# Performance work log

Measured on AMD Instinct MI355X. Metric: run time of the kernel, lower is better.

## Reference

```python
import jax, jax.numpy as jnp
import numpy as np
import math

CS = 8       # cell_size
NBINS = 8
SIGMA = 1.0
IMG = 224
BATCH = 256
TWO_PI = 2.0 * math.pi


def setup_inputs() -> dict:
    key = jax.random.key(0)
    x = jax.random.normal(key, (BATCH, 3, IMG, IMG), dtype=jnp.float32)
    coords = jnp.arange(CS, dtype=jnp.float32) - (CS - 1) / 2.0
    xx, yy = jnp.meshgrid(coords, coords, indexing='ij')
    gauss = jnp.exp(-(xx ** 2 + yy ** 2) / (2.0 * SIGMA ** 2)).reshape(1, CS * CS)
    kx = jnp.array([[-1., 0., 1.], [-2., 0., 2.], [-1., 0., 1.]], dtype=jnp.float32).reshape(1, 1, 3, 3)
    ky = jnp.array([[-1., -2., -1.], [0., 0., 0.], [1., 2., 1.]], dtype=jnp.float32).reshape(1, 1, 3, 3)
    return {"x": x, "gauss": gauss, "kx": kx, "ky": ky}


def _conv(im, k):
    # NCHW conv, padding=1, stride=1 (matches F.conv2d(..., padding=1))
    return jax.lax.conv_general_dilated(
        im, k, window_strides=(1, 1), padding=[(1, 1), (1, 1)],
        dimension_numbers=('NCHW', 'OIHW', 'NCHW'))


def reference(x, gauss, kx, ky):
    bs, _, H, W = x.shape
    gray = 0.2989 * x[:, 0:1] + 0.587 * x[:, 1:2] + 0.114 * x[:, 2:3]  # [bs,1,H,W]
    gx = _conv(gray, kx)
    gy = _conv(gray, ky)
    mag = jnp.sqrt(gx ** 2 + gy ** 2 + 1e-6)
    ang = jnp.mod(jnp.arctan2(gy, gx), TWO_PI)
    Hc, Wc = H // CS, W // CS
    n_cells = Hc * Wc

    def to_cells(a):
        # [bs,1,H,W] -> [bs*n_cells, CS*CS], within-cell order (kh,kw) row-major
        # matching F.unfold's kernel-position ordering.
        return a.reshape(bs, Hc, CS, Wc, CS).transpose(0, 1, 3, 2, 4).reshape(bs * n_cells, CS * CS)

    mags = to_cells(mag) * gauss  # gauss broadcasts over kernel positions
    angs = to_cells(ang)

    bin_w = TWO_PI / NBINS
    idx = (angs / bin_w).astype(jnp.int32) % NBINS  # [bs*n_cells, CS*CS]

    N = bs * n_cells
    hist = jnp.zeros((N, NBINS), dtype=mags.dtype)
    hist = hist.at[jnp.arange(N)[:, None], idx].add(mags)  # scatter_add per cell
    hist = hist.reshape(bs, n_cells * NBINS)
    hist = hist / (jnp.linalg.norm(hist, axis=1, keepdims=True) + 1e-6)
    return hist
```

## Files before the change

kernel.cpp:

```cpp
#include <hip/hip_runtime.h>
#include <math.h>

#define CS 8
#define NBINS 8
#define IMG 224
#define HC 28
#define OUTPER (HC*HC*NBINS)
#define BATCH 256
#define RS 16
#define GR (RS + 2)
#define GSTRIDE 232
#define GOFF 4

__global__ void hog_zero_kernel(float* __restrict__ sumsq) {
    if (threadIdx.x < BATCH) sumsq[threadIdx.x] = 0.f;
}

__global__ __launch_bounds__(256) void hog_hist_kernel(
    const float* __restrict__ x, const float* __restrict__ gauss,
    float* __restrict__ out, float* __restrict__ sumsq)
{
    const int b   = blockIdx.x;
    const int by  = blockIdx.y;
    const int tid = threadIdx.x;
    const int r0  = by * RS;

    __shared__ float g[GR][GSTRIDE];
    __shared__ float wsum[4];

    const size_t plane = (size_t)IMG * IMG;
    const float* xb = x + (size_t)b * 3 * plane;

    if (tid < GR * 2) {
        int rr = tid >> 1, cc = (tid & 1) ? (GOFF + IMG) : (GOFF - 1);
        g[rr][cc] = 0.f;
    }

    for (int idx = tid; idx < GR * (IMG / 4); idx += 256) {
        int row = idx / (IMG / 4), c4 = idx % (IMG / 4);
        int gr = r0 - 1 + row;
        float4 val = make_float4(0.f, 0.f, 0.f, 0.f);
        if (gr >= 0 && gr < IMG) {
            const float* base = xb + (size_t)gr * IMG;
            float4 R = ((const float4*)base)[c4];
            float4 G = ((const float4*)(base + plane))[c4];
            float4 B = ((const float4*)(base + 2 * plane))[c4];
            val.x = 0.2989f * R.x + 0.587f * G.x + 0.114f * B.x;
            val.y = 0.2989f * R.y + 0.587f * G.y + 0.114f * B.y;
            val.z = 0.2989f * R.z + 0.587f * G.z + 0.114f * B.z;
            val.w = 0.2989f * R.w + 0.587f * G.w + 0.114f * B.w;
        }
        *(float4*)&g[row][GOFF + c4 * 4] = val;
    }
    __syncthreads();

    float ssq = 0.f;
    if (tid < IMG) {
        const int c  = tid;
        const int wc = c & 7;

        float wgt[8];
        #pragma unroll
        for (int i = 0; i < 8; ++i) wgt[i] = gauss[i * 8 + wc];

        float h[8];
        #pragma unroll
        for (int k = 0; k < 8; ++k) h[k] = 0.f;

        auto dump = [&](int crow) {
            #pragma unroll
            for (int s = 1; s < 8; s <<= 1) {
                #pragma unroll
                for (int k = 0; k < 8; ++k) h[k] += __shfl_xor(h[k], s, 64);
            }
            float v = (wc < 4) ? ((wc < 2) ? (wc == 0 ? h[0] : h[1])
                                          : (wc == 2 ? h[2] : h[3]))
                               : ((wc < 6) ? (wc == 4 ? h[4] : h[5])
                                          : (wc == 6 ? h[6] : h[7]));
            out[(size_t)b * OUTPER + (size_t)crow * (HC * NBINS) + c] = v;
            ssq += v * v;
            #pragma unroll
            for (int k = 0; k < 8; ++k) h[k] = 0.f;
        };

        float t0 = g[0][c + 3], t1 = g[0][c + 4], t2 = g[0][c + 5];
        float m0 = g[1][c + 3], m1 = g[1][c + 4], m2 = g[1][c + 5];

        #pragma unroll
        for (int sr = 0; sr < RS; ++sr) {
            float b0 = g[sr + 2][c + 3], b1 = g[sr + 2][c + 4], b2 = g[sr + 2][c + 5];
            float gx = (t2 - t0) + 2.f * (m2 - m0) + (b2 - b0);
            float gy = (b0 - t0) + 2.f * (b1 - t1) + (b2 - t2);
            float mag = sqrtf(gx * gx + gy * gy + 1e-6f);
            float ax = fabsf(gx), ay = fabsf(gy);

            int bin;
            if (gy > 0.f)       bin = (gx > 0.f)  ? ((gy < gx) ? 0 : 1)
                                    : (gx == 0.f) ? 2 : ((ay > ax) ? 2 : 3);
            else if (gy == 0.f) bin = (gx < 0.f) ? 4 : 0;
            else                bin = (gx < 0.f)  ? ((ay < ax) ? 4 : 5)
                                    : (gx == 0.f) ? 6 : ((ay > ax) ? 6 : 7);

            float wm = wgt[sr & 7] * mag;
            #pragma unroll
            for (int k = 0; k < 8; ++k) h[k] += (bin == k) ? wm : 0.f;

            t0 = m0; t1 = m1; t2 = m2;
            m0 = b0; m1 = b1; m2 = b2;

            if (sr == 7)       dump(2 * by);
            else if (sr == 15) dump(2 * by + 1);
        }
    }

    #pragma unroll
    for (int o = 32; o > 0; o >>= 1) ssq += __shfl_down(ssq, o, 64);
    if ((tid & 63) == 0) wsum[tid >> 6] = ssq;
    __syncthreads();
    if (tid == 0) atomicAdd(&sumsq[b], wsum[0] + wsum[1] + wsum[2] + wsum[3]);
}

__global__ __launch_bounds__(256) void hog_norm_kernel(
    float* __restrict__ out, const float* __restrict__ sumsq)
{
    int i = blockIdx.x * blockDim.x + threadIdx.x;
    const int vec_per_img = OUTPER / 4;
    if (i >= BATCH * vec_per_img) return;
    int b = i / vec_per_img;
    float n = sqrtf(sumsq[b]) + 1e-6f;
    float4* o4 = (float4*)out;
    float4 v = o4[i];
    v.x /= n; v.y /= n; v.z /= n; v.w /= n;
    o4[i] = v;
}

extern "C" void kernel_launch(void* const* d_in, const int* in_sizes, int n_in,
                              void* d_out, int out_size, void* d_ws, size_t ws_size,
                              hipStream_t stream) {
    const float* x     = (const float*)d_in[0];
    const float* gauss = (const float*)d_in[1];
    float* out   = (float*)d_out;
    float* sumsq = (float*)d_ws;

    hog_zero_kernel<<<1, 256, 0, stream>>>(sumsq);
    dim3 grid(BATCH, IMG / RS);
    hog_hist_kernel<<<grid, 256, 0, stream>>>(x, gauss, out, sumsq);
    hog_norm_kernel<<<(BATCH * OUTPER / 4 + 255) / 256, 256, 0, stream>>>(out, sumsq);
}
```

Baseline: 244.4 us.

## Split grayscale into separate pass, double row strip height, use reciprocal normalization

Adds a standalone kernel that converts RGB to grayscale into workspace memory and also zeroes the per-image sum-of-squares, so the histogram kernel reads one gray plane instead of three colour planes. The histogram kernel now processes 32-row strips, halving the grid and the relative halo overhead, and loads tiles with a fixed unrolled loop using clamped addresses. Normalization multiplies by a reciprocal instead of dividing. The cost is an extra full-size gray write and read through global memory, plus fewer blocks per image.

Result: slower. 261.4 us (+7.0%).

```diff
diff --git a/kernel.cpp b/kernel.cpp
--- a/kernel.cpp
+++ b/kernel.cpp
@@ -7,17 +7,34 @@
 #define HC 28
 #define OUTPER (HC*HC*NBINS)
 #define BATCH 256
-#define RS 16
+#define P4 (IMG*IMG/4)
+#define RS 32
 #define GR (RS + 2)
 #define GSTRIDE 232
 #define GOFF 4
 
-__global__ void hog_zero_kernel(float* __restrict__ sumsq) {
-    if (threadIdx.x < BATCH) sumsq[threadIdx.x] = 0.f;
+__global__ __launch_bounds__(256) void hog_gray_kernel(
+    const float4* __restrict__ x, float4* __restrict__ gray,
+    float* __restrict__ sumsq)
+{
+    if (blockIdx.x == 0) sumsq[threadIdx.x] = 0.f;
+    int p = blockIdx.x * 256 + threadIdx.x;
+    int b = p / P4;
+    int i = p - b * P4;
+    const float4* xb = x + (size_t)b * 3 * P4;
+    float4 R = xb[i];
+    float4 G = xb[P4 + i];
+    float4 B = xb[2 * P4 + i];
+    float4 g;
+    g.x = 0.2989f * R.x + 0.587f * G.x + 0.114f * B.x;
+    g.y = 0.2989f * R.y + 0.587f * G.y + 0.114f * B.y;
+    g.z = 0.2989f * R.z + 0.587f * G.z + 0.114f * B.z;
+    g.w = 0.2989f * R.w + 0.587f * G.w + 0.114f * B.w;
+    gray[p] = g;
 }
 
 __global__ __launch_bounds__(256) void hog_hist_kernel(
-    const float* __restrict__ x, const float* __restrict__ gauss,
+    const float* __restrict__ gray, const float* __restrict__ gauss,
     float* __restrict__ out, float* __restrict__ sumsq)
 {
     const int b   = blockIdx.x;
@@ -28,29 +45,22 @@
     __shared__ float g[GR][GSTRIDE];
     __shared__ float wsum[4];
 
-    const size_t plane = (size_t)IMG * IMG;
-    const float* xb = x + (size_t)b * 3 * plane;
-
     if (tid < GR * 2) {
         int rr = tid >> 1, cc = (tid & 1) ? (GOFF + IMG) : (GOFF - 1);
         g[rr][cc] = 0.f;
     }
 
-    for (int idx = tid; idx < GR * (IMG / 4); idx += 256) {
-        int row = idx / (IMG / 4), c4 = idx % (IMG / 4);
-        int gr = r0 - 1 + row;
-        float4 val = make_float4(0.f, 0.f, 0.f, 0.f);
-        if (gr >= 0 && gr < IMG) {
-            const float* base = xb + (size_t)gr * IMG;
-            float4 R = ((const float4*)base)[c4];
-            float4 G = ((const float4*)(base + plane))[c4];
-            float4 B = ((const float4*)(base + 2 * plane))[c4];
-            val.x = 0.2989f * R.x + 0.587f * G.x + 0.114f * B.x;
-            val.y = 0.2989f * R.y + 0.587f * G.y + 0.114f * B.y;
-            val.z = 0.2989f * R.z + 0.587f * G.z + 0.114f * B.z;
-            val.w = 0.2989f * R.w + 0.587f * G.w + 0.114f * B.w;
-        }
-        *(float4*)&g[row][GOFF + c4 * 4] = val;
+    const float4* gb = (const float4*)(gray + (size_t)b * IMG * IMG);
+    #pragma unroll
+    for (int k = 0; k < 8; ++k) {
+        int idx = tid + k * 256;
+        int ii  = idx < GR * 56 ? idx : GR * 56 - 1;
+        int row = ii / 56, c4 = ii - row * 56;
+        int gr  = r0 - 1 + row;
+        int grc = gr < 0 ? 0 : (gr > IMG - 1 ? IMG - 1 : gr);
+        float4 v = gb[grc * 56 + c4];
+        if (gr < 0 || gr >= IMG) v = make_float4(0.f, 0.f, 0.f, 0.f);
+        if (idx < GR * 56) *(float4*)&g[row][GOFF + c4 * 4] = v;
     }
     __syncthreads();
 
@@ -108,8 +118,7 @@
             t0 = m0; t1 = m1; t2 = m2;
             m0 = b0; m1 = b1; m2 = b2;
 
-            if (sr == 7)       dump(2 * by);
-            else if (sr == 15) dump(2 * by + 1);
+            if ((sr & 7) == 7) dump(4 * by + (sr >> 3));
         }
     }
 
@@ -127,10 +136,10 @@
     const int vec_per_img = OUTPER / 4;
     if (i >= BATCH * vec_per_img) return;
     int b = i / vec_per_img;
-    float n = sqrtf(sumsq[b]) + 1e-6f;
+    float inv = 1.0f / (sqrtf(sumsq[b]) + 1e-6f);
     float4* o4 = (float4*)out;
     float4 v = o4[i];
-    v.x /= n; v.y /= n; v.z /= n; v.w /= n;
+    v.x *= inv; v.y *= inv; v.z *= inv; v.w *= inv;
     o4[i] = v;
 }
 
@@ -141,9 +150,11 @@
     const float* gauss = (const float*)d_in[1];
     float* out   = (float*)d_out;
     float* sumsq = (float*)d_ws;
+    float* gray  = (float*)d_ws + 256;
 
-    hog_zero_kernel<<<1, 256, 0, stream>>>(sumsq);
+    hog_gray_kernel<<<BATCH * P4 / 256, 256, 0, stream>>>(
+        (const float4*)x, (float4*)gray, sumsq);
     dim3 grid(BATCH, IMG / RS);
-    hog_hist_kernel<<<grid, 256, 0, stream>>>(x, gauss, out, sumsq);
+    hog_hist_kernel<<<grid, 256, 0, stream>>>(gray, gauss, out, sumsq);
     hog_norm_kernel<<<(BATCH * OUTPER / 4 + 255) / 256, 256, 0, stream>>>(out, sumsq);
 }
```

## Stream 56-row strips through ring buffer with prefetched loads, drop atomics

Applied to the files above, without the earlier changes.

Each block now handles a 56-row strip (7 cell rows) instead of 16 rows, using a 16-slot ring buffer in shared memory. While the current cell row is being computed, the next 8 gray rows are loaded into registers and written into the ring afterwards. This cuts halo reloads from 18/16 to 58/56 rows and overlaps global loads with compute. The per-image sum-of-squares now goes into per-strip partial slots instead of atomics, removing the zero kernel, and the norm kernel multiplies by a reciprocal. The trade-offs are fewer blocks (1024 instead of 3584), an extra barrier per cell row, and higher register pressure.

After: 236.5 us. 1.03x faster.

```diff
diff --git a/kernel.cpp b/kernel.cpp
--- a/kernel.cpp
+++ b/kernel.cpp
@@ -1,115 +1,146 @@
 #include <hip/hip_runtime.h>
 #include <math.h>
 
-#define CS 8
 #define NBINS 8
 #define IMG 224
 #define HC 28
 #define OUTPER (HC*HC*NBINS)
 #define BATCH 256
-#define RS 16
-#define GR (RS + 2)
+#define PL4 12544
 #define GSTRIDE 232
 #define GOFF 4
+#define SLOTS 16
 
-__global__ void hog_zero_kernel(float* __restrict__ sumsq) {
-    if (threadIdx.x < BATCH) sumsq[threadIdx.x] = 0.f;
-}
+__global__ __launch_bounds__(256) void hog_main_kernel(
+    const float4* __restrict__ x, const float* __restrict__ gauss,
+    float* __restrict__ out, float* __restrict__ partial)
+{
+    const int b     = blockIdx.x;
+    const int by    = blockIdx.y;
+    const int tid   = threadIdx.x;
+    const int rbase = by * 56;
 
-__global__ __launch_bounds__(256) void hog_hist_kernel(
-    const float* __restrict__ x, const float* __restrict__ gauss,
-    float* __restrict__ out, float* __restrict__ sumsq)
-{
-    const int b   = blockIdx.x;
-    const int by  = blockIdx.y;
-    const int tid = threadIdx.x;
-    const int r0  = by * RS;
-
-    __shared__ float g[GR][GSTRIDE];
+    __shared__ float g[SLOTS][GSTRIDE];
     __shared__ float wsum[4];
 
-    const size_t plane = (size_t)IMG * IMG;
-    const float* xb = x + (size_t)b * 3 * plane;
+    const float4* xb = x + (size_t)b * 3 * PL4;
 
-    if (tid < GR * 2) {
+    if (tid < SLOTS * 2) {
         int rr = tid >> 1, cc = (tid & 1) ? (GOFF + IMG) : (GOFF - 1);
         g[rr][cc] = 0.f;
     }
 
-    for (int idx = tid; idx < GR * (IMG / 4); idx += 256) {
-        int row = idx / (IMG / 4), c4 = idx % (IMG / 4);
-        int gr = r0 - 1 + row;
-        float4 val = make_float4(0.f, 0.f, 0.f, 0.f);
-        if (gr >= 0 && gr < IMG) {
-            const float* base = xb + (size_t)gr * IMG;
-            float4 R = ((const float4*)base)[c4];
-            float4 G = ((const float4*)(base + plane))[c4];
-            float4 B = ((const float4*)(base + 2 * plane))[c4];
-            val.x = 0.2989f * R.x + 0.587f * G.x + 0.114f * B.x;
-            val.y = 0.2989f * R.y + 0.587f * G.y + 0.114f * B.y;
-            val.z = 0.2989f * R.z + 0.587f * G.z + 0.114f * B.z;
-            val.w = 0.2989f * R.w + 0.587f * G.w + 0.114f * B.w;
+    {
+        float4 R[3], G[3], B[3];
+        int gr[3], c4[3]; bool act[3];
+        #pragma unroll
+        for (int k = 0; k < 3; ++k) {
+            int idx = tid + k * 256;
+            act[k] = idx < 560;
+            int ii = act[k] ? idx : 0;
+            int row = ii / 56; c4[k] = ii - row * 56;
+            gr[k] = rbase - 1 + row;
+            int grc = gr[k] < 0 ? 0 : (gr[k] > IMG - 1 ? IMG - 1 : gr[k]);
+            const float4* p = xb + grc * 56 + c4[k];
+            R[k] = p[0]; G[k] = p[PL4]; B[k] = p[2 * PL4];
         }
-        *(float4*)&g[row][GOFF + c4 * 4] = val;
+        #pragma unroll
+        for (int k = 0; k < 3; ++k) if (act[k]) {
+            bool z = (gr[k] < 0) || (gr[k] > IMG - 1);
+            float4 v;
+            v.x = z ? 0.f : 0.2989f * R[k].x + 0.587f * G[k].x + 0.114f * B[k].x;
+            v.y = z ? 0.f : 0.2989f * R[k].y + 0.587f * G[k].y + 0.114f * B[k].y;
+            v.z = z ? 0.f : 0.2989f * R[k].z + 0.587f * G[k].z + 0.114f * B[k].z;
+            v.w = z ? 0.f : 0.2989f * R[k].w + 0.587f * G[k].w + 0.114f * B[k].w;
+            *(float4*)&g[gr[k] & (SLOTS - 1)][GOFF + 4 * c4[k]] = v;
+        }
     }
     __syncthreads();
 
+    const int c = tid, wc = tid & 7;
+    float wgt[8];
+    #pragma unroll
+    for (int i = 0; i < 8; ++i) wgt[i] = gauss[i * 8 + wc];
     float ssq = 0.f;
-    if (tid < IMG) {
-        const int c  = tid;
-        const int wc = c & 7;
 
-        float wgt[8];
-        #pragma unroll
-        for (int i = 0; i < 8; ++i) wgt[i] = gauss[i * 8 + wc];
+    for (int s = 0; s < 7; ++s) {
+        float4 Rp[2], Gp[2], Bp[2];
+        int pgr[2], pc4[2]; bool pact[2];
+        if (s < 6) {
+            #pragma unroll
+            for (int k = 0; k < 2; ++k) {
+                int idx = tid + k * 256;
+                pact[k] = idx < 448;
+                int ii = pact[k] ? idx : 0;
+                int row = ii / 56; pc4[k] = ii - row * 56;
+                pgr[k] = rbase + 8 * s + 9 + row;
+                int grc = pgr[k] > IMG - 1 ? IMG - 1 : pgr[k];
+                const float4* p = xb + grc * 56 + pc4[k];
+                Rp[k] = p[0]; Gp[k] = p[PL4]; Bp[k] = p[2 * PL4];
+            }
+        }
 
-        float h[8];
-        #pragma unroll
-        for (int k = 0; k < 8; ++k) h[k] = 0.f;
+        if (tid < IMG) {
+            const int r0 = rbase + 8 * s;
+            float h[8];
+            #pragma unroll
+            for (int k = 0; k < 8; ++k) h[k] = 0.f;
 
-        auto dump = [&](int crow) {
+            int st = (r0 - 1) & (SLOTS - 1), sm = r0 & (SLOTS - 1);
+            float t0 = g[st][c + 3], t1 = g[st][c + 4], t2 = g[st][c + 5];
+            float m0 = g[sm][c + 3], m1 = g[sm][c + 4], m2 = g[sm][c + 5];
+
             #pragma unroll
-            for (int s = 1; s < 8; s <<= 1) {
+            for (int sr = 0; sr < 8; ++sr) {
+                int sb = (r0 + sr + 1) & (SLOTS - 1);
+                float b0 = g[sb][c + 3], b1 = g[sb][c + 4], b2 = g[sb][c + 5];
+                float gx = (t2 - t0) + 2.f * (m2 - m0) + (b2 - b0);
+                float gy = (b0 - t0) + 2.f * (b1 - t1) + (b2 - t2);
+                float mag = sqrtf(gx * gx + gy * gy + 1e-6f);
+                float ax = fabsf(gx), ay = fabsf(gy);
+
+                int bin;
+                if (gy > 0.f)       bin = (gx > 0.f)  ? ((gy < gx) ? 0 : 1)
+                                        : (gx == 0.f) ? 2 : ((ay > ax) ? 2 : 3);
+                else if (gy == 0.f) bin = (gx < 0.f) ? 4 : 0;
+                else                bin = (gx < 0.f)  ? ((ay < ax) ? 4 : 5)
+                                        : (gx == 0.f) ? 6 : ((ay > ax) ? 6 : 7);
+
+                float wm = wgt[sr] * mag;
                 #pragma unroll
-                for (int k = 0; k < 8; ++k) h[k] += __shfl_xor(h[k], s, 64);
+                for (int k = 0; k < 8; ++k) h[k] += (bin == k) ? wm : 0.f;
+
+                t0 = m0; t1 = m1; t2 = m2;
+                m0 = b0; m1 = b1; m2 = b2;
+            }
+
+            #pragma unroll
+            for (int sh = 1; sh < 8; sh <<= 1) {
+                #pragma unroll
+                for (int k = 0; k < 8; ++k) h[k] += __shfl_xor(h[k], sh, 64);
             }
             float v = (wc < 4) ? ((wc < 2) ? (wc == 0 ? h[0] : h[1])
                                           : (wc == 2 ? h[2] : h[3]))
                                : ((wc < 6) ? (wc == 4 ? h[4] : h[5])
                                           : (wc == 6 ? h[6] : h[7]));
+            int crow = by * 7 + s;
             out[(size_t)b * OUTPER + (size_t)crow * (HC * NBINS) + c] = v;
             ssq += v * v;
+        }
+        __syncthreads();
+
+        if (s < 6) {
             #pragma unroll
-            for (int k = 0; k < 8; ++k) h[k] = 0.f;
-        };
-
-        float t0 = g[0][c + 3], t1 = g[0][c + 4], t2 = g[0][c + 5];
-        float m0 = g[1][c + 3], m1 = g[1][c + 4], m2 = g[1][c + 5];
-
-        #pragma unroll
-        for (int sr = 0; sr < RS; ++sr) {
-            float b0 = g[sr + 2][c + 3], b1 = g[sr + 2][c + 4], b2 = g[sr + 2][c + 5];
-            float gx = (t2 - t0) + 2.f * (m2 - m0) + (b2 - b0);
-            float gy = (b0 - t0) + 2.f * (b1 - t1) + (b2 - t2);
-            float mag = sqrtf(gx * gx + gy * gy + 1e-6f);
-            float ax = fabsf(gx), ay = fabsf(gy);
-
-            int bin;
-            if (gy > 0.f)       bin = (gx > 0.f)  ? ((gy < gx) ? 0 : 1)
-                                    : (gx == 0.f) ? 2 : ((ay > ax) ? 2 : 3);
-            else if (gy == 0.f) bin = (gx < 0.f) ? 4 : 0;
-            else                bin = (gx < 0.f)  ? ((ay < ax) ? 4 : 5)
-                                    : (gx == 0.f) ? 6 : ((ay > ax) ? 6 : 7);
-
-            float wm = wgt[sr & 7] * mag;
-            #pragma unroll
-            for (int k = 0; k < 8; ++k) h[k] += (bin == k) ? wm : 0.f;
-
-            t0 = m0; t1 = m1; t2 = m2;
-            m0 = b0; m1 = b1; m2 = b2;
-
-            if (sr == 7)       dump(2 * by);
-            else if (sr == 15) dump(2 * by + 1);
+            for (int k = 0; k < 2; ++k) if (pact[k]) {
+                bool z = pgr[k] > IMG - 1;
+                float4 v;
+                v.x = z ? 0.f : 0.2989f * Rp[k].x + 0.587f * Gp[k].x + 0.114f * Bp[k].x;
+                v.y = z ? 0.f : 0.2989f * Rp[k].y + 0.587f * Gp[k].y + 0.114f * Bp[k].y;
+                v.z = z ? 0.f : 0.2989f * Rp[k].z + 0.587f * Gp[k].z + 0.114f * Bp[k].z;
+                v.w = z ? 0.f : 0.2989f * Rp[k].w + 0.587f * Gp[k].w + 0.114f * Bp[k].w;
+                *(float4*)&g[pgr[k] & (SLOTS - 1)][GOFF + 4 * pc4[k]] = v;
+            }
+            __syncthreads();
         }
     }
 
@@ -117,20 +148,22 @@
     for (int o = 32; o > 0; o >>= 1) ssq += __shfl_down(ssq, o, 64);
     if ((tid & 63) == 0) wsum[tid >> 6] = ssq;
     __syncthreads();
-    if (tid == 0) atomicAdd(&sumsq[b], wsum[0] + wsum[1] + wsum[2] + wsum[3]);
+    if (tid == 0) partial[by * BATCH + b] = wsum[0] + wsum[1] + wsum[2] + wsum[3];
 }
 
 __global__ __launch_bounds__(256) void hog_norm_kernel(
-    float* __restrict__ out, const float* __restrict__ sumsq)
+    float* __restrict__ out, const float* __restrict__ partial)
 {
     int i = blockIdx.x * blockDim.x + threadIdx.x;
     const int vec_per_img = OUTPER / 4;
     if (i >= BATCH * vec_per_img) return;
     int b = i / vec_per_img;
-    float n = sqrtf(sumsq[b]) + 1e-6f;
+    float s = partial[b] + partial[BATCH + b] + partial[2 * BATCH + b]
+            + partial[3 * BATCH + b];
+    float inv = 1.0f / (sqrtf(s) + 1e-6f);
     float4* o4 = (float4*)out;
     float4 v = o4[i];
-    v.x /= n; v.y /= n; v.z /= n; v.w /= n;
+    v.x *= inv; v.y *= inv; v.z *= inv; v.w *= inv;
     o4[i] = v;
 }
 
@@ -139,11 +172,11 @@
                               hipStream_t stream) {
     const float* x     = (const float*)d_in[0];
     const float* gauss = (const float*)d_in[1];
-    float* out   = (float*)d_out;
-    float* sumsq = (float*)d_ws;
+    float* out     = (float*)d_out;
+    float* partial = (float*)d_ws;
 
-    hog_zero_kernel<<<1, 256, 0, stream>>>(sumsq);
-    dim3 grid(BATCH, IMG / RS);
-    hog_hist_kernel<<<grid, 256, 0, stream>>>(x, gauss, out, sumsq);
-    hog_norm_kernel<<<(BATCH * OUTPER / 4 + 255) / 256, 256, 0, stream>>>(out, sumsq);
+    dim3 grid(BATCH, 4);
+    hog_main_kernel<<<grid, 256, 0, stream>>>(
+        (const float4*)x, gauss, out, partial);
+    hog_norm_kernel<<<(BATCH * OUTPER / 4 + 255) / 256, 256, 0, stream>>>(out, partial);
 }
```

## Assign one cell row per wave, drop atomics and zero kernel

Applied to the files above, without the earlier changes.

Restructures the histogram kernel so each 64-lane wave owns one 8-row cell strip with its own LDS tile, using wave barriers instead of block syncs. Every column is handled by a lane across four chunks, so all 64 lanes stay busy rather than only 224 of 256 threads. Per-strip sums of squares are written to a partial buffer rather than accumulated with atomics, which removes the zeroing kernel. The normalization kernel runs one block per image, reduces the partials and multiplies by a reciprocal. In exchange, halo rows are now re-read for every 8-row strip instead of every 16 rows, which adds more redundant input loads.

Result: slower. 252.8 us (+3.5%).

```diff
diff --git a/kernel.cpp b/kernel.cpp
--- a/kernel.cpp
+++ b/kernel.cpp
@@ -1,94 +1,82 @@
 #include <hip/hip_runtime.h>
 #include <math.h>
 
-#define CS 8
 #define NBINS 8
 #define IMG 224
 #define HC 28
 #define OUTPER (HC*HC*NBINS)
 #define BATCH 256
-#define RS 16
-#define GR (RS + 2)
-#define GSTRIDE 232
+#define PL4 12544
+#define WROWS 10
+#define WSTRIDE 232
 #define GOFF 4
 
-__global__ void hog_zero_kernel(float* __restrict__ sumsq) {
-    if (threadIdx.x < BATCH) sumsq[threadIdx.x] = 0.f;
-}
+__global__ __launch_bounds__(256) void hog_main_kernel(
+    const float4* __restrict__ x, const float* __restrict__ gauss,
+    float* __restrict__ out, float* __restrict__ partial)
+{
+    __shared__ float g[4][WROWS][WSTRIDE];
+    const int tid  = threadIdx.x;
+    const int wv   = tid >> 6;
+    const int lane = tid & 63;
+    const int gw   = blockIdx.x * 4 + wv;
+    const int b    = gw / HC;
+    const int cr   = gw - b * HC;
+    const int r0   = cr * 8;
 
-__global__ __launch_bounds__(256) void hog_hist_kernel(
-    const float* __restrict__ x, const float* __restrict__ gauss,
-    float* __restrict__ out, float* __restrict__ sumsq)
-{
-    const int b   = blockIdx.x;
-    const int by  = blockIdx.y;
-    const int tid = threadIdx.x;
-    const int r0  = by * RS;
+    const float4* xb = x + (size_t)b * 3 * PL4;
 
-    __shared__ float g[GR][GSTRIDE];
-    __shared__ float wsum[4];
-
-    const size_t plane = (size_t)IMG * IMG;
-    const float* xb = x + (size_t)b * 3 * plane;
-
-    if (tid < GR * 2) {
-        int rr = tid >> 1, cc = (tid & 1) ? (GOFF + IMG) : (GOFF - 1);
-        g[rr][cc] = 0.f;
+    if (lane < WROWS * 2) {
+        int rr = lane >> 1, cc = (lane & 1) ? (GOFF + IMG) : (GOFF - 1);
+        g[wv][rr][cc] = 0.f;
     }
 
-    for (int idx = tid; idx < GR * (IMG / 4); idx += 256) {
-        int row = idx / (IMG / 4), c4 = idx % (IMG / 4);
+    #pragma unroll 3
+    for (int k = 0; k < 9; ++k) {
+        int idx = k * 64 + lane;
+        bool act = idx < 560;
+        int ii = act ? idx : 559;
+        int row = ii / 56, c4 = ii - row * 56;
         int gr = r0 - 1 + row;
-        float4 val = make_float4(0.f, 0.f, 0.f, 0.f);
-        if (gr >= 0 && gr < IMG) {
-            const float* base = xb + (size_t)gr * IMG;
-            float4 R = ((const float4*)base)[c4];
-            float4 G = ((const float4*)(base + plane))[c4];
-            float4 B = ((const float4*)(base + 2 * plane))[c4];
-            val.x = 0.2989f * R.x + 0.587f * G.x + 0.114f * B.x;
-            val.y = 0.2989f * R.y + 0.587f * G.y + 0.114f * B.y;
-            val.z = 0.2989f * R.z + 0.587f * G.z + 0.114f * B.z;
-            val.w = 0.2989f * R.w + 0.587f * G.w + 0.114f * B.w;
-        }
-        *(float4*)&g[row][GOFF + c4 * 4] = val;
+        int grc = gr < 0 ? 0 : (gr > IMG - 1 ? IMG - 1 : gr);
+        const float4* p = xb + grc * 56 + c4;
+        float4 R = p[0];
+        float4 G = p[PL4];
+        float4 B = p[2 * PL4];
+        bool z = (gr < 0) || (gr > IMG - 1);
+        float4 v;
+        v.x = z ? 0.f : 0.2989f * R.x + 0.587f * G.x + 0.114f * B.x;
+        v.y = z ? 0.f : 0.2989f * R.y + 0.587f * G.y + 0.114f * B.y;
+        v.z = z ? 0.f : 0.2989f * R.z + 0.587f * G.z + 0.114f * B.z;
+        v.w = z ? 0.f : 0.2989f * R.w + 0.587f * G.w + 0.114f * B.w;
+        if (act) *(float4*)&g[wv][row][GOFF + 4 * c4] = v;
     }
-    __syncthreads();
+    __builtin_amdgcn_wave_barrier();
+
+    const int wc = lane & 7;
+    float wgt[8];
+    #pragma unroll
+    for (int i = 0; i < 8; ++i) wgt[i] = gauss[i * 8 + wc];
 
     float ssq = 0.f;
-    if (tid < IMG) {
-        const int c  = tid;
-        const int wc = c & 7;
+    const size_t obase = (size_t)b * OUTPER + (size_t)cr * IMG;
 
-        float wgt[8];
-        #pragma unroll
-        for (int i = 0; i < 8; ++i) wgt[i] = gauss[i * 8 + wc];
+    for (int ch = 0; ch < 4; ++ch) {
+        int c = ch * 64 + lane;
+        bool act = c < IMG;
+        int cc = act ? c : IMG - 1;
 
         float h[8];
         #pragma unroll
-        for (int k = 0; k < 8; ++k) h[k] = 0.f;
+        for (int k2 = 0; k2 < 8; ++k2) h[k2] = 0.f;
 
-        auto dump = [&](int crow) {
-            #pragma unroll
-            for (int s = 1; s < 8; s <<= 1) {
-                #pragma unroll
-                for (int k = 0; k < 8; ++k) h[k] += __shfl_xor(h[k], s, 64);
-            }
-            float v = (wc < 4) ? ((wc < 2) ? (wc == 0 ? h[0] : h[1])
-                                          : (wc == 2 ? h[2] : h[3]))
-                               : ((wc < 6) ? (wc == 4 ? h[4] : h[5])
-                                          : (wc == 6 ? h[6] : h[7]));
-            out[(size_t)b * OUTPER + (size_t)crow * (HC * NBINS) + c] = v;
-            ssq += v * v;
-            #pragma unroll
-            for (int k = 0; k < 8; ++k) h[k] = 0.f;
-        };
-
-        float t0 = g[0][c + 3], t1 = g[0][c + 4], t2 = g[0][c + 5];
-        float m0 = g[1][c + 3], m1 = g[1][c + 4], m2 = g[1][c + 5];
+        float t0 = g[wv][0][cc + 3], t1 = g[wv][0][cc + 4], t2 = g[wv][0][cc + 5];
+        float m0 = g[wv][1][cc + 3], m1 = g[wv][1][cc + 4], m2 = g[wv][1][cc + 5];
 
         #pragma unroll
-        for (int sr = 0; sr < RS; ++sr) {
-            float b0 = g[sr + 2][c + 3], b1 = g[sr + 2][c + 4], b2 = g[sr + 2][c + 5];
+        for (int sr = 0; sr < 8; ++sr) {
+            float b0 = g[wv][sr + 2][cc + 3], b1 = g[wv][sr + 2][cc + 4],
+                  b2 = g[wv][sr + 2][cc + 5];
             float gx = (t2 - t0) + 2.f * (m2 - m0) + (b2 - b0);
             float gy = (b0 - t0) + 2.f * (b1 - t1) + (b2 - t2);
             float mag = sqrtf(gx * gx + gy * gy + 1e-6f);
@@ -101,37 +89,53 @@
             else                bin = (gx < 0.f)  ? ((ay < ax) ? 4 : 5)
                                     : (gx == 0.f) ? 6 : ((ay > ax) ? 6 : 7);
 
-            float wm = wgt[sr & 7] * mag;
+            float wm = wgt[sr] * mag;
             #pragma unroll
-            for (int k = 0; k < 8; ++k) h[k] += (bin == k) ? wm : 0.f;
+            for (int k2 = 0; k2 < 8; ++k2) h[k2] += (bin == k2) ? wm : 0.f;
 
             t0 = m0; t1 = m1; t2 = m2;
             m0 = b0; m1 = b1; m2 = b2;
+        }
 
-            if (sr == 7)       dump(2 * by);
-            else if (sr == 15) dump(2 * by + 1);
+        #pragma unroll
+        for (int sh = 1; sh < 8; sh <<= 1) {
+            #pragma unroll
+            for (int k2 = 0; k2 < 8; ++k2) h[k2] += __shfl_xor(h[k2], sh, 64);
+        }
+        float v = (wc < 4) ? ((wc < 2) ? (wc == 0 ? h[0] : h[1])
+                                      : (wc == 2 ? h[2] : h[3]))
+                           : ((wc < 6) ? (wc == 4 ? h[4] : h[5])
+                                      : (wc == 6 ? h[6] : h[7]));
+        if (act) {
+            out[obase + c] = v;
+            ssq += v * v;
         }
     }
 
     #pragma unroll
     for (int o = 32; o > 0; o >>= 1) ssq += __shfl_down(ssq, o, 64);
-    if ((tid & 63) == 0) wsum[tid >> 6] = ssq;
-    __syncthreads();
-    if (tid == 0) atomicAdd(&sumsq[b], wsum[0] + wsum[1] + wsum[2] + wsum[3]);
+    if (lane == 0) partial[gw] = ssq;
 }
 
-__global__ __launch_bounds__(256) void hog_norm_kernel(
-    float* __restrict__ out, const float* __restrict__ sumsq)
+__global__ __launch_bounds__(512) void hog_norm_kernel(
+    float* __restrict__ out, const float* __restrict__ partial)
 {
-    int i = blockIdx.x * blockDim.x + threadIdx.x;
-    const int vec_per_img = OUTPER / 4;
-    if (i >= BATCH * vec_per_img) return;
-    int b = i / vec_per_img;
-    float n = sqrtf(sumsq[b]) + 1e-6f;
-    float4* o4 = (float4*)out;
-    float4 v = o4[i];
-    v.x /= n; v.y /= n; v.z /= n; v.w /= n;
-    o4[i] = v;
+    const int b = blockIdx.x;
+    __shared__ float s_inv;
+    if (threadIdx.x < 64) {
+        float s = (threadIdx.x < HC) ? partial[b * HC + threadIdx.x] : 0.f;
+        #pragma unroll
+        for (int o = 16; o > 0; o >>= 1) s += __shfl_down(s, o, 64);
+        if (threadIdx.x == 0) s_inv = 1.0f / (sqrtf(s) + 1e-6f);
+    }
+    __syncthreads();
+    float inv = s_inv;
+    float4* o4 = (float4*)(out + (size_t)b * OUTPER);
+    for (int i = threadIdx.x; i < OUTPER / 4; i += 512) {
+        float4 v = o4[i];
+        v.x *= inv; v.y *= inv; v.z *= inv; v.w *= inv;
+        o4[i] = v;
+    }
 }
 
 extern "C" void kernel_launch(void* const* d_in, const int* in_sizes, int n_in,
@@ -139,11 +143,10 @@
                               hipStream_t stream) {
     const float* x     = (const float*)d_in[0];
     const float* gauss = (const float*)d_in[1];
-    float* out   = (float*)d_out;
-    float* sumsq = (float*)d_ws;
+    float* out     = (float*)d_out;
+    float* partial = (float*)d_ws;
 
-    hog_zero_kernel<<<1, 256, 0, stream>>>(sumsq);
-    dim3 grid(BATCH, IMG / RS);
-    hog_hist_kernel<<<grid, 256, 0, stream>>>(x, gauss, out, sumsq);
-    hog_norm_kernel<<<(BATCH * OUTPER / 4 + 255) / 256, 256, 0, stream>>>(out, sumsq);
+    hog_main_kernel<<<BATCH * HC / 4, 256, 0, stream>>>(
+        (const float4*)x, gauss, out, partial);
+    hog_norm_kernel<<<BATCH, 512, 0, stream>>>(out, partial);
 }
```
